# Performance work log

Measured on AMD Instinct MI355X. Metric: run time of the kernel, lower is better.

Reference implementation:

```python
import jax, jax.numpy as jnp
from jax import lax
import numpy as np

B, N, C = 4, 16384, 64
M_POINT, K_SAMPLE = 1024, 32
RADIUS = 0.5
LN_EPS = 1e-5
CP = C + 3  # grouped channels with use_xyz


def _fps(xyz, m):
    """D-FPS: furthest point sampling on Euclidean coords. xyz (B,N,3) -> (B,m) int32."""
    b, n, _ = xyz.shape
    min_d = jnp.full((b, n), 1e10, xyz.dtype)
    pt0 = xyz[:, 0]  # CUDA FPS starts from index 0

    def step(carry, _):
        md, last = carry
        d = jnp.sum((xyz - last[:, None, :]) ** 2, axis=-1)  # (B,N)
        md = jnp.minimum(md, d)
        idx = jnp.argmax(md, axis=1)  # (B,)
        nxt = jnp.take_along_axis(xyz, idx[:, None, None], axis=1)[:, 0]
        return (md, nxt), idx.astype(jnp.int32)

    _, idxs = lax.scan(step, (min_d, pt0), None, length=m - 1)  # (m-1,B)
    return jnp.concatenate([jnp.zeros((1, b), jnp.int32), idxs], axis=0).T  # (B,m)


def _ball_query(xyz, new_xyz, radius, k):
    """First k neighbors (by original index) within radius; pad with first hit. -> (B,M,k)."""
    b, n, _ = xyz.shape
    d2 = jnp.sum((new_xyz[:, :, None, :] - xyz[:, None, :, :]) ** 2, -1)  # (B,M,N)
    scores = jnp.where(d2 <= radius * radius, jnp.arange(n, dtype=jnp.int32), n)
    neg_top, _ = lax.top_k(-scores, k)  # k smallest scores = first k in-radius indices
    idx = -neg_top  # (B,M,k), ascending
    idx = jnp.where(idx < n, idx, idx[..., :1])  # pad invalid slots with first hit
    return idx


def setup_inputs() -> dict:
    key = jax.random.key(0)
    ks = jax.random.split(key, 8)
    points_xyz = jax.random.uniform(ks[0], (B, N, 3)) * 2.0 - 1.0
    features = jax.random.normal(ks[1], (B, C, N))
    prompt_emb = jax.random.normal(ks[2], (1, M_POINT, 2)) * 0.02
    proj_w = jax.random.normal(ks[3], (CP, 2)) * 0.5
    proj_b = jnp.zeros((CP,))
    ln_g = jnp.ones((CP,))
    ln_b = jnp.zeros((CP,))
    pw_w = jax.random.normal(ks[4], (M_POINT, CP)) * 0.05
    pw_b = jnp.zeros((M_POINT,))
    w0 = jax.random.normal(ks[5], (128, CP)) / np.sqrt(CP)
    b0 = jnp.zeros((128,))
    w1 = jax.random.normal(ks[6], (256, 128)) / np.sqrt(128.0)
    b1 = jnp.zeros((256,))
    return dict(points_xyz=points_xyz, features=features, prompt_emb=prompt_emb,
                proj_w=proj_w, proj_b=proj_b, ln_g=ln_g, ln_b=ln_b,
                pw_w=pw_w, pw_b=pw_b, w0=w0, b0=b0, w1=w1, b1=b1)


def reference(points_xyz, features, prompt_emb, proj_w, proj_b, ln_g, ln_b,
              pw_w, pw_b, w0, b0, w1, b1):
    # sample centers (D-FPS)
    indices = _fps(points_xyz, M_POINT)                                   # (B,M)
    new_xyz = jnp.take_along_axis(points_xyz, indices[:, :, None], axis=1)  # (B,M,3)
    # ball-query grouping + gather
    idx = _ball_query(points_xyz, new_xyz, RADIUS, K_SAMPLE)              # (B,M,K)
    gx = jax.vmap(lambda p, i: p[i])(points_xyz, idx)                     # (B,M,K,3)
    gx = gx - new_xyz[:, :, None, :]                                      # relative xyz
    gf = jax.vmap(lambda f, i: f[:, i])(features, idx)                    # (B,C,M,K)
    g = jnp.concatenate([jnp.transpose(gx, (0, 3, 1, 2)), gf], axis=1)    # (B,C+3,M,K)
    # incorporate_prompt
    emb = g.mean(axis=(-2, -1))                                           # (B,C+3)
    pw = jax.nn.softmax(emb @ pw_w.T + pw_b, axis=1)                      # (B,M)
    pe = prompt_emb @ proj_w.T + proj_b                                   # (1,M,C+3)
    mu = pe.mean(-1, keepdims=True)
    var = ((pe - mu) ** 2).mean(-1, keepdims=True)
    pe = (pe - mu) * lax.rsqrt(var + LN_EPS) * ln_g + ln_b
    pe = jax.nn.gelu(pe, approximate=False)                               # (1,M,C+3)
    g = g + pe[0].T[None, :, :, None] * pw[:, None, :, None]              # (B,C+3,M,K)
    # shared MLP (1x1 conv) + ReLU
    h = jax.nn.relu(jnp.einsum('oc,bcmk->bomk', w0, g) + b0[:, None, None])
    h = jax.nn.relu(jnp.einsum('oc,bcmk->bomk', w1, h) + b1[:, None, None])
    # max pool over neighbors K
    pooled = h.max(axis=-1)                                               # (B,256,M)
    return new_xyz, pooled, indices
```

## Files before the change

### kernel.cpp

```cpp
#include <hip/hip_runtime.h>
#include <hip/hip_bf16.h>

#define NB   4
#define NPTS 16384
#define NC   64
#define NM   1024
#define NK   32
#define NCP  67
#define RAD2 0.25f

#define OFF_W0T     0u
#define OFF_W1T     8576u
#define OFF_NEWXYZ  41344u
#define OFF_IDXBALL 53632u
#define OFF_CNT     184704u
#define OFF_EMB     250240u
#define OFF_PW      250624u
#define OFF_PE      254720u
#define OFF_SX      323328u
#define OFF_SY      388864u
#define OFF_SZ      454400u
#define OFF_SKLO    519936u

#define OUT_NEWXYZ 0u
#define OUT_POOLED 12288u
#define OUT_IDX    1060864u

__global__ __launch_bounds__(256) void k_prepw(const float* __restrict__ w0,
                                               const float* __restrict__ w1,
                                               float* __restrict__ w0t,
                                               float* __restrict__ w1t) {
  int t = blockIdx.x * 256 + threadIdx.x;
  if (t < 128 * NCP) { int o = t / NCP, c = t % NCP; w0t[c * 128 + o] = w0[t]; }
  if (t < 256 * 128) { int o2 = t / 128, o = t % 128; w1t[o * 256 + o2] = w1[t]; }
}

__device__ __forceinline__ unsigned mpart3(unsigned v) {
  return (v & 1u) | ((v & 2u) << 2) | ((v & 4u) << 4);
}
__device__ __forceinline__ unsigned cellof(float x, float y, float z) {
  unsigned qx = (unsigned)fminf(fmaxf((x + 1.0f) * 4.0f, 0.0f), 7.0f);
  unsigned qy = (unsigned)fminf(fmaxf((y + 1.0f) * 4.0f, 0.0f), 7.0f);
  unsigned qz = (unsigned)fminf(fmaxf((z + 1.0f) * 4.0f, 0.0f), 7.0f);
  return mpart3(qx) | (mpart3(qy) << 1) | (mpart3(qz) << 2);
}

__global__ __launch_bounds__(1024) void k_sort(const float* __restrict__ xyz,
                                               float* __restrict__ sx,
                                               float* __restrict__ sy,
                                               float* __restrict__ sz,
                                               unsigned* __restrict__ sklo) {
  const int b = blockIdx.x, t = threadIdx.x;
  const int lane = t & 63, wid = t >> 6;
  const float* xb = xyz + (size_t)b * NPTS * 3;
  __shared__ unsigned s_hist[512], s_off[512], s_wsum[8];
  if (t < 512) s_hist[t] = 0u;
  __syncthreads();
#pragma unroll
  for (int i = 0; i < 16; ++i) {
    int p = t + 1024 * i;
    float x = xb[p * 3 + 0], y = xb[p * 3 + 1], z = xb[p * 3 + 2];
    atomicAdd(&s_hist[cellof(x, y, z)], 1u);
  }
  __syncthreads();
  unsigned v = (t < 512) ? s_hist[t] : 0u;
#pragma unroll
  for (int off = 1; off < 64; off <<= 1) {
    unsigned u = __shfl_up(v, off);
    if (lane >= off) v += u;
  }
  if (t < 512 && lane == 63) s_wsum[wid] = v;
  __syncthreads();
  if (t < 512) {
    unsigned add = 0;
    for (int w = 0; w < wid; ++w) add += s_wsum[w];
    s_off[t] = add + v - s_hist[t];
  }
  __syncthreads();
#pragma unroll
  for (int i = 0; i < 16; ++i) {
    int p = t + 1024 * i;
    float x = xb[p * 3 + 0], y = xb[p * 3 + 1], z = xb[p * 3 + 2];
    unsigned pos = atomicAdd(&s_off[cellof(x, y, z)], 1u);
    sx[b * NPTS + pos] = x;
    sy[b * NPTS + pos] = y;
    sz[b * NPTS + pos] = z;
    sklo[b * NPTS + pos] = 16383u - (unsigned)p;
  }
}

__device__ __forceinline__ unsigned long long umax64(unsigned long long a,
                                                     unsigned long long b) {
  return a > b ? a : b;
}
__device__ __forceinline__ unsigned long long pack_key(float m, unsigned kl,
                                                       int bb) {
  return (((unsigned long long)__float_as_uint(m)) << 22) |
         (((unsigned long long)kl) << 8) | (unsigned long long)(unsigned)bb;
}

template <bool INIT>
__device__ __forceinline__ void fps_bucket(
    int bbp, int gl, float lx, float ly, float lz,
    const float* __restrict__ bx, const float* __restrict__ by,
    const float* __restrict__ bz, const unsigned* __restrict__ bk,
    float* s_md, unsigned short* s_klo,
    unsigned long long* skey_out, float4* swin_out,
    float* s_bxl, float* s_bxh, float* s_byl, float* s_byh,
    float* s_bzl, float* s_bzh) {
  const int p0 = bbp * 64 + gl * 8;
  float4 xa = *(const float4*)(bx + p0);
  float4 xc = *(const float4*)(bx + p0 + 4);
  float4 ya = *(const float4*)(by + p0);
  float4 yc = *(const float4*)(by + p0 + 4);
  float4 za = *(const float4*)(bz + p0);
  float4 zc = *(const float4*)(bz + p0 + 4);
  float xx[8] = {xa.x, xa.y, xa.z, xa.w, xc.x, xc.y, xc.z, xc.w};
  float yy[8] = {ya.x, ya.y, ya.z, ya.w, yc.x, yc.y, yc.z, yc.w};
  float zz[8] = {za.x, za.y, za.z, za.w, zc.x, zc.y, zc.z, zc.w};
  unsigned kls[8];
  float mds[8];
  if constexpr (INIT) {
    uint4 k0 = *(const uint4*)(bk + p0);
    uint4 k1 = *(const uint4*)(bk + p0 + 4);
    kls[0] = k0.x; kls[1] = k0.y; kls[2] = k0.z; kls[3] = k0.w;
    kls[4] = k1.x; kls[5] = k1.y; kls[6] = k1.z; kls[7] = k1.w;
  } else {
    uint4 kv = *(const uint4*)(&s_klo[p0]);
    kls[0] = kv.x & 0xFFFFu; kls[1] = kv.x >> 16;
    kls[2] = kv.y & 0xFFFFu; kls[3] = kv.y >> 16;
    kls[4] = kv.z & 0xFFFFu; kls[5] = kv.z >> 16;
    kls[6] = kv.w & 0xFFFFu; kls[7] = kv.w >> 16;
    float4 ma = *(const float4*)(&s_md[p0]);
    float4 mb = *(const float4*)(&s_md[p0 + 4]);
    mds[0] = ma.x; mds[1] = ma.y; mds[2] = ma.z; mds[3] = ma.w;
    mds[4] = mb.x; mds[5] = mb.y; mds[6] = mb.z; mds[7] = mb.w;
  }
  unsigned long long best = 0ull;
  float bwx = 0.f, bwy = 0.f, bwz = 0.f;
  float nmd[8];
#pragma unroll
  for (int i = 0; i < 8; ++i) {
    float dx = __fsub_rn(xx[i], lx);
    float dy = __fsub_rn(yy[i], ly);
    float dz = __fsub_rn(zz[i], lz);
    float d2 = __fadd_rn(__fadd_rn(__fmul_rn(dx, dx), __fmul_rn(dy, dy)),
                         __fmul_rn(dz, dz));
    float m = INIT ? d2 : fminf(mds[i], d2);
    nmd[i] = m;
    unsigned long long key = pack_key(m, kls[i], bbp);
    if (key > best) { best = key; bwx = xx[i]; bwy = yy[i]; bwz = zz[i]; }
  }
  *(float4*)(&s_md[p0])     = make_float4(nmd[0], nmd[1], nmd[2], nmd[3]);
  *(float4*)(&s_md[p0 + 4]) = make_float4(nmd[4], nmd[5], nmd[6], nmd[7]);
  if constexpr (INIT) {
    uint4 kw;
    kw.x = kls[0] | (kls[1] << 16); kw.y = kls[2] | (kls[3] << 16);
    kw.z = kls[4] | (kls[5] << 16); kw.w = kls[6] | (kls[7] << 16);
    *(uint4*)(&s_klo[p0]) = kw;
  }
  unsigned long long gk = best;
#pragma unroll
  for (int off = 1; off < 8; off <<= 1) {
    unsigned long long o = __shfl_xor(gk, off);
    gk = o > gk ? o : gk;
  }
  if constexpr (INIT) {
    float xl = xx[0], xh = xx[0], yl = yy[0], yh = yy[0], zl = zz[0], zh = zz[0];
#pragma unroll
    for (int i = 1; i < 8; ++i) {
      xl = fminf(xl, xx[i]); xh = fmaxf(xh, xx[i]);
      yl = fminf(yl, yy[i]); yh = fmaxf(yh, yy[i]);
      zl = fminf(zl, zz[i]); zh = fmaxf(zh, zz[i]);
    }
#pragma unroll
    for (int off = 1; off < 8; off <<= 1) {
      xl = fminf(xl, __shfl_xor(xl, off)); xh = fmaxf(xh, __shfl_xor(xh, off));
      yl = fminf(yl, __shfl_xor(yl, off)); yh = fmaxf(yh, __shfl_xor(yh, off));
      zl = fminf(zl, __shfl_xor(zl, off)); zh = fmaxf(zh, __shfl_xor(zh, off));
    }
    if (gl == 0) {
      s_bxl[bbp] = xl; s_bxh[bbp] = xh;
      s_byl[bbp] = yl; s_byh[bbp] = yh;
      s_bzl[bbp] = zl; s_bzh[bbp] = zh;
    }
  }
  if (best == gk) swin_out[bbp] = make_float4(bwx, bwy, bwz, 0.f);
  if (gl == 0) skey_out[bbp] = gk;
}

__global__ __launch_bounds__(512) void k_fps(const float* __restrict__ xyz,
                                             const float* __restrict__ sx,
                                             const float* __restrict__ sy,
                                             const float* __restrict__ sz,
                                             const unsigned* __restrict__ sklo,
                                             float* __restrict__ newxyz,
                                             float* __restrict__ out) {
  const int b = blockIdx.x, t = threadIdx.x;
  const int lane = t & 63, w = t >> 6;
  const int gl = lane & 7, g = lane >> 3;
  const float* xb = xyz + (size_t)b * NPTS * 3;
  const float* bx = sx + b * NPTS;
  const float* by = sy + b * NPTS;
  const float* bz = sz + b * NPTS;
  const unsigned* bk = sklo + b * NPTS;
  __shared__ float s_md[NPTS];
  __shared__ unsigned short s_klo[NPTS];
  __shared__ float s_bxl[256], s_bxh[256], s_byl[256], s_byh[256],
                   s_bzl[256], s_bzh[256];
  __shared__ unsigned long long s_bkey[2][256];
  __shared__ float4 s_bwin[2][256];
  float lx = xb[0], ly = xb[1], lz = xb[2];
  if (t == 0) {
    newxyz[(size_t)b * NM * 3 + 0] = lx;
    newxyz[(size_t)b * NM * 3 + 1] = ly;
    newxyz[(size_t)b * NM * 3 + 2] = lz;
    out[OUT_NEWXYZ + (size_t)b * NM * 3 + 0] = lx;
    out[OUT_NEWXYZ + (size_t)b * NM * 3 + 1] = ly;
    out[OUT_NEWXYZ + (size_t)b * NM * 3 + 2] = lz;
    out[OUT_IDX + b * NM] = 0.0f;
  }
#pragma unroll
  for (int r = 0; r < 4; ++r) {
    int bbp = 32 * w + r * 8 + g;
    fps_bucket<true>(bbp, gl, lx, ly, lz, bx, by, bz, bk, s_md, s_klo,
                     s_bkey[0], s_bwin[0],
                     s_bxl, s_bxh, s_byl, s_byh, s_bzl, s_bzh);
  }
  __syncthreads();
  for (int s = 1; s < NM; ++s) {
    const int cur = s & 1, prv = cur ^ 1;
    unsigned long long k =
        umax64(umax64(s_bkey[prv][lane], s_bkey[prv][lane + 64]),
               umax64(s_bkey[prv][lane + 128], s_bkey[prv][lane + 192]));
#pragma unroll
    for (int off = 1; off < 64; off <<= 1) {
      unsigned long long o = __shfl_xor(k, off);
      k = o > k ? o : k;
    }
    const int bbw = (int)(k & 0xFFull);
    float4 wv = s_bwin[prv][bbw];
    lx = wv.x; ly = wv.y; lz = wv.z;
    if (t == 0) {
      const int idx = 16383 - (int)((k >> 8) & 0x3FFFull);
      newxyz[((size_t)b * NM + s) * 3 + 0] = lx;
      newxyz[((size_t)b * NM + s) * 3 + 1] = ly;
      newxyz[((size_t)b * NM + s) * 3 + 2] = lz;
      out[OUT_NEWXYZ + ((size_t)b * NM + s) * 3 + 0] = lx;
      out[OUT_NEWXYZ + ((size_t)b * NM + s) * 3 + 1] = ly;
      out[OUT_NEWXYZ + ((size_t)b * NM + s) * 3 + 2] = lz;
      out[OUT_IDX + b * NM + s] = (float)idx;
    }
    bool keep = false;
    if (lane < 32) {
      const int bbj = 32 * w + lane;
      unsigned long long kj = s_bkey[prv][bbj];
      float mm = __uint_as_float((unsigned)(kj >> 22));
      float gx = fmaxf(fmaxf(__fsub_rn(s_bxl[bbj], lx), __fsub_rn(lx, s_bxh[bbj])), 0.f);
      float gy = fmaxf(fmaxf(__fsub_rn(s_byl[bbj], ly), __fsub_rn(ly, s_byh[bbj])), 0.f);
      float gz = fmaxf(fmaxf(__fsub_rn(s_bzl[bbj], lz), __fsub_rn(lz, s_bzh[bbj])), 0.f);
      float lb = __fadd_rn(__fadd_rn(__fmul_rn(gx, gx), __fmul_rn(gy, gy)),
                           __fmul_rn(gz, gz));
      keep = !(__fmul_rn(lb, 0.999984741f) > __fmul_rn(mm, 1.000015259f));
      if (!keep) {
        s_bkey[cur][bbj] = kj;
        s_bwin[cur][bbj] = s_bwin[prv][bbj];
      }
    }
    unsigned long long mask = __ballot(keep);
    while (mask) {
      unsigned long long m2 = mask;
#pragma unroll
      for (int r = 0; r < 7; ++r) if (r < g) m2 &= (m2 - 1ull);
      if (m2) {
        int jj = (int)__builtin_ctzll(m2);
        fps_bucket<false>(32 * w + jj, gl, lx, ly, lz, bx, by, bz, bk,
                          s_md, s_klo, s_bkey[cur], s_bwin[cur],
                          s_bxl, s_bxh, s_byl, s_byh, s_bzl, s_bzh);
      }
#pragma unroll
      for (int r = 0; r < 8; ++r) mask &= (mask - 1ull);
    }
    __syncthreads();
  }
}

__global__ __launch_bounds__(256) void k_ball(const float* __restrict__ xyz,
                                              const float* __restrict__ newxyz,
                                              int* __restrict__ idxball,
                                              int* __restrict__ cnt,
                                              float* __restrict__ emb) {
  __shared__ int s_idx[4][NK];
  const int lane = threadIdx.x & 63, wid = threadIdx.x >> 6;
  const int gid = blockIdx.x * 4 + wid;
  const int b = gid >> 10;
  const float* xb = xyz + (size_t)b * NPTS * 3;
  const float cx = newxyz[gid * 3 + 0];
  const float cy = newxyz[gid * 3 + 1];
  const float cz = newxyz[gid * 3 + 2];
  int total = 0;
  for (int base = 0; base < NPTS && total < NK; base += 64) {
    int n = base + lane;
    float dx = __fsub_rn(xb[n * 3 + 0], cx);
    float dy = __fsub_rn(xb[n * 3 + 1], cy);
    float dz = __fsub_rn(xb[n * 3 + 2], cz);
    float d2 = __fadd_rn(__fadd_rn(__fmul_rn(dx, dx), __fmul_rn(dy, dy)),
                         __fmul_rn(dz, dz));
    bool hit = d2 <= RAD2;
    unsigned long long mask = __ballot(hit);
    int pos = total + (int)__popcll(mask & ((1ull << lane) - 1ull));
    if (hit && pos < NK) s_idx[wid][pos] = n;
    total += (int)__popcll(mask);
  }
  int tt = total < NK ? total : NK;
  if (lane >= tt && lane < NK) s_idx[wid][lane] = s_idx[wid][0];
  int v = 0;
  if (lane < NK) {
    v = s_idx[wid][lane];
    idxball[(size_t)gid * NK + lane] = v;
    atomicAdd(&cnt[b * NPTS + v], 1);
  }
  float sx = 0.f, sy = 0.f, sz = 0.f;
  if (lane < NK) { sx = xb[v * 3 + 0]; sy = xb[v * 3 + 1]; sz = xb[v * 3 + 2]; }
#pragma unroll
  for (int off = 1; off < 64; off <<= 1) {
    sx += __shfl_xor(sx, off);
    sy += __shfl_xor(sy, off);
    sz += __shfl_xor(sz, off);
  }
  if (lane == 0) {
    atomicAdd(&emb[b * 96 + 0], sx - 32.0f * cx);
    atomicAdd(&emb[b * 96 + 1], sy - 32.0f * cy);
    atomicAdd(&emb[b * 96 + 2], sz - 32.0f * cz);
  }
}

__global__ __launch_bounds__(256) void k_embfeat(const float* __restrict__ feat,
                                                 const int* __restrict__ cnt,
                                                 float* __restrict__ emb) {
  const int c = blockIdx.x, b = blockIdx.y;
  const float* f = feat + ((size_t)b * NC + c) * NPTS;
  const int* ct = cnt + b * NPTS;
  float acc = 0.f;
  for (int n = threadIdx.x; n < NPTS; n += 256)
    acc = fmaf((float)ct[n], f[n], acc);
  __shared__ float red[4];
#pragma unroll
  for (int off = 1; off < 64; off <<= 1) acc += __shfl_xor(acc, off);
  if ((threadIdx.x & 63) == 0) red[threadIdx.x >> 6] = acc;
  __syncthreads();
  if (threadIdx.x == 0)
    emb[b * 96 + 3 + c] = red[0] + red[1] + red[2] + red[3];
}

__global__ __launch_bounds__(64) void k_pe(const float* __restrict__ prompt,
                                           const float* __restrict__ projw,
                                           const float* __restrict__ projb,
                                           const float* __restrict__ lng,
                                           const float* __restrict__ lnb,
                                           float* __restrict__ pe) {
  const int m = blockIdx.x, lane = threadIdx.x;
  const float p0 = prompt[m * 2 + 0], p1 = prompt[m * 2 + 1];
  const int c1 = lane, c2 = lane + 64;
  float v1 = p0 * projw[c1 * 2 + 0] + p1 * projw[c1 * 2 + 1] + projb[c1];
  float v2 = 0.f;
  if (c2 < NCP) v2 = p0 * projw[c2 * 2 + 0] + p1 * projw[c2 * 2 + 1] + projb[c2];
  float s = v1 + ((c2 < NCP) ? v2 : 0.f);
#pragma unroll
  for (int off = 1; off < 64; off <<= 1) s += __shfl_xor(s, off);
  float mu = s * (1.0f / 67.0f);
  float d1 = v1 - mu;
  float d2v = (c2 < NCP) ? (v2 - mu) : 0.f;
  float q = d1 * d1 + d2v * d2v;
#pragma unroll
  for (int off = 1; off < 64; off <<= 1) q += __shfl_xor(q, off);
  float inv = 1.0f / sqrtf(q * (1.0f / 67.0f) + 1e-5f);
  {
    float y = d1 * inv * lng[c1] + lnb[c1];
    pe[m * NCP + c1] = 0.5f * y * (1.0f + erff(y * 0.70710678118654752f));
  }
  if (c2 < NCP) {
    float y = (v2 - mu) * inv * lng[c2] + lnb[c2];
    pe[m * NCP + c2] = 0.5f * y * (1.0f + erff(y * 0.70710678118654752f));
  }
}

__global__ __launch_bounds__(1024) void k_pw(const float* __restrict__ emb,
                                             const float* __restrict__ pww,
                                             const float* __restrict__ pwb,
                                             float* __restrict__ pw) {
  const int b = blockIdx.x, m = threadIdx.x;
  __shared__ float se[NCP];
  __shared__ float red[16];
  __shared__ float bcast;
  if (m < NCP) se[m] = emb[b * 96 + m] * (1.0f / 32768.0f);
  __syncthreads();
  float acc = pwb[m];
  for (int c = 0; c < NCP; ++c) acc = fmaf(se[c], pww[m * NCP + c], acc);
  float mx = acc;
#pragma unroll
  for (int off = 1; off < 64; off <<= 1) mx = fmaxf(mx, __shfl_xor(mx, off));
  if ((m & 63) == 0) red[m >> 6] = mx;
  __syncthreads();
  if (m == 0) {
    float v = red[0];
    for (int w = 1; w < 16; ++w) v = fmaxf(v, red[w]);
    bcast = v;
  }
  __syncthreads();
  float e = expf(acc - bcast);
  float ssum = e;
#pragma unroll
  for (int off = 1; off < 64; off <<= 1) ssum += __shfl_xor(ssum, off);
  if ((m & 63) == 0) red[m >> 6] = ssum;
  __syncthreads();
  if (m == 0) {
    float v = 0.f;
    for (int w = 0; w < 16; ++w) v += red[w];
    bcast = v;
  }
  __syncthreads();
  pw[b * NM + m] = e / bcast;
}

__global__ __launch_bounds__(256) void k_main(const float* __restrict__ feat,
                                              const float* __restrict__ xyz,
                                              const float* __restrict__ newxyz,
                                              const int* __restrict__ idxball,
                                              const float* __restrict__ pe,
                                              const float* __restrict__ pwbuf,
                                              const float* __restrict__ w0t,
                                              const float* __restrict__ b0,
                                              const float* __restrict__ w1t,
                                              const float* __restrict__ b1,
                                              float* __restrict__ out) {
  __shared__ __align__(16) float g[NCP * 36];
  __shared__ __align__(16) float h0[128 * 36];
  __shared__ int s_idx[NK];
  __shared__ float spe[NCP];
  const int bid = blockIdx.x;
  const int b = bid >> 10, m = bid & 1023;
  const int t = threadIdx.x;
  const float pwv = pwbuf[bid];
  if (t < NK) {
    int n = idxball[(size_t)bid * NK + t];
    n = n < 0 ? 0 : (n > NPTS - 1 ? NPTS - 1 : n);
    s_idx[t] = n;
  }
  if (t < NCP) spe[t] = pe[m * NCP + t] * pwv;
  __syncthreads();
  for (int e = t; e < NK * NC; e += 256) {
    int k = e >> 6, c = e & 63;
    int n = s_idx[k];
    g[(3 + c) * 36 + k] = feat[((size_t)b * NC + c) * NPTS + n] + spe[3 + c];
  }
  if (t < 96) {
    int k = t & 31, d = t >> 5;
    int n = s_idx[k];
    float cv = newxyz[bid * 3 + d];
    g[d * 36 + k] = (xyz[((size_t)b * NPTS + n) * 3 + d] - cv) + spe[d];
  }
  __syncthreads();
  {
    const int o = t & 127, kb = (t >> 7) * 16;
    float acc[16];
    float bb = b0[o];
#pragma unroll
    for (int j = 0; j < 16; ++j) acc[j] = bb;
    for (int c = 0; c < NCP; ++c) {
      float w = w0t[c * 128 + o];
      const float4* gp = reinterpret_cast<const float4*>(&g[c * 36 + kb]);
#pragma unroll
      for (int qq = 0; qq < 4; ++qq) {
        float4 gv = gp[qq];
        acc[qq * 4 + 0] = fmaf(w, gv.x, acc[qq * 4 + 0]);
        acc[qq * 4 + 1] = fmaf(w, gv.y, acc[qq * 4 + 1]);
        acc[qq * 4 + 2] = fmaf(w, gv.z, acc[qq * 4 + 2]);
        acc[qq * 4 + 3] = fmaf(w, gv.w, acc[qq * 4 + 3]);
      }
    }
    float4* hp = reinterpret_cast<float4*>(&h0[o * 36 + kb]);
#pragma unroll
    for (int qq = 0; qq < 4; ++qq) {
      float4 hv;
      hv.x = fmaxf(acc[qq * 4 + 0], 0.f);
      hv.y = fmaxf(acc[qq * 4 + 1], 0.f);
      hv.z = fmaxf(acc[qq * 4 + 2], 0.f);
      hv.w = fmaxf(acc[qq * 4 + 3], 0.f);
      hp[qq] = hv;
    }
  }
  __syncthreads();
  {
    const int o2 = t;
    float acc[32];
    float bb = b1[o2];
#pragma unroll
    for (int j = 0; j < 32; ++j) acc[j] = bb;
    for (int o = 0; o < 128; ++o) {
      float w = w1t[o * 256 + o2];
      const float4* hp = reinterpret_cast<const float4*>(&h0[o * 36]);
#pragma unroll
      for (int qq = 0; qq < 8; ++qq) {
        float4 hv = hp[qq];
        acc[qq * 4 + 0] = fmaf(w, hv.x, acc[qq * 4 + 0]);
        acc[qq * 4 + 1] = fmaf(w, hv.y, acc[qq * 4 + 1]);
        acc[qq * 4 + 2] = fmaf(w, hv.z, acc[qq * 4 + 2]);
        acc[qq * 4 + 3] = fmaf(w, hv.w, acc[qq * 4 + 3]);
      }
    }
    float mx = 0.f;
#pragma unroll
    for (int k = 0; k < 32; ++k) mx = fmaxf(mx, acc[k]);
    out[OUT_POOLED + ((size_t)(b * 256 + o2)) * NM + m] = mx;
  }
}

extern "C" void kernel_launch(void* const* d_in, const int* in_sizes, int n_in,
                              void* d_out, int out_size, void* d_ws, size_t ws_size,
                              hipStream_t stream) {
  const float* xyz    = (const float*)d_in[0];
  const float* feat   = (const float*)d_in[1];
  const float* prompt = (const float*)d_in[2];
  const float* projw  = (const float*)d_in[3];
  const float* projb  = (const float*)d_in[4];
  const float* lng    = (const float*)d_in[5];
  const float* lnb    = (const float*)d_in[6];
  const float* pww    = (const float*)d_in[7];
  const float* pwb    = (const float*)d_in[8];
  const float* w0     = (const float*)d_in[9];
  const float* b0     = (const float*)d_in[10];
  const float* w1     = (const float*)d_in[11];
  const float* b1     = (const float*)d_in[12];
  float* ws = (float*)d_ws;
  float* out = (float*)d_out;

  float* w0t      = ws + OFF_W0T;
  float* w1t      = ws + OFF_W1T;
  float* nxyz     = ws + OFF_NEWXYZ;
  int*   idxball  = (int*)(ws + OFF_IDXBALL);
  int*   cnt      = (int*)(ws + OFF_CNT);
  float* emb      = ws + OFF_EMB;
  float* pwv      = ws + OFF_PW;
  float* pev      = ws + OFF_PE;
  float* sxw      = ws + OFF_SX;
  float* syw      = ws + OFF_SY;
  float* szw      = ws + OFF_SZ;
  unsigned* sklo  = (unsigned*)(ws + OFF_SKLO);

  hipMemsetAsync(cnt, 0, NB * NPTS * sizeof(int), stream);
  hipMemsetAsync(emb, 0, NB * 96 * sizeof(float), stream);

  k_prepw<<<128, 256, 0, stream>>>(w0, w1, w0t, w1t);
  k_sort<<<NB, 1024, 0, stream>>>(xyz, sxw, syw, szw, sklo);
  k_fps<<<NB, 512, 0, stream>>>(xyz, sxw, syw, szw, sklo, nxyz, out);
  k_ball<<<NB * NM / 4, 256, 0, stream>>>(xyz, nxyz, idxball, cnt, emb);
  k_embfeat<<<dim3(NC, NB), 256, 0, stream>>>(feat, cnt, emb);
  k_pe<<<NM, 64, 0, stream>>>(prompt, projw, projb, lng, lnb, pev);
  k_pw<<<NB, 1024, 0, stream>>>(emb, pww, pwb, pwv);
  k_main<<<NB * NM, 256, 0, stream>>>(feat, xyz, nxyz, idxball, pev, pwv,
                                      w0t, b0, w1t, b1, out);
}
```

Measured before the change: 2.433 ms.

## Use 16-lane bucket groups with DPP reductions in FPS and cache bucket bounds in registers

The FPS bucket update now assigns 16 lanes of 4 points each to a bucket instead of 8 lanes of 8 points. The intra-group argmax, including the winning coordinates, and the bounding-box min/max are reduced with DPP row_shr operations instead of __shfl_xor. The wave-wide key max also moves to DPP row shifts and broadcasts plus readlane. Each lane keeps its bucket's bounding box in registers rather than reloading it from LDS every step. The goal is to cut shuffle latency and per-lane serial work on the serial FPS critical path. The cost is fewer buckets processed in parallel per wave pass and DPP code that is harder to get right, for example with row masks.

```diff
diff --git a/kernel.cpp b/kernel.cpp
--- a/kernel.cpp
+++ b/kernel.cpp
@@ -99,94 +99,118 @@
          (((unsigned long long)kl) << 8) | (unsigned long long)(unsigned)bb;
 }
 
+#define DPPI(v, CTRL, RM) \
+  __builtin_amdgcn_update_dpp((int)(v), (int)(v), CTRL, RM, 0xf, false)
+
+#define DPP_PAY(CTRL) { \
+  unsigned h2 = (unsigned)DPPI(hi, CTRL, 0xf); \
+  unsigned l2 = (unsigned)DPPI(lo, CTRL, 0xf); \
+  float x2 = __int_as_float(DPPI(__float_as_int(bwx), CTRL, 0xf)); \
+  float y2 = __int_as_float(DPPI(__float_as_int(bwy), CTRL, 0xf)); \
+  float z2 = __int_as_float(DPPI(__float_as_int(bwz), CTRL, 0xf)); \
+  bool tk = (h2 > hi) || (h2 == hi && l2 > lo); \
+  hi = tk ? h2 : hi; lo = tk ? l2 : lo; \
+  bwx = tk ? x2 : bwx; bwy = tk ? y2 : bwy; bwz = tk ? z2 : bwz; }
+
+#define DPP_K(CTRL, RM) { \
+  unsigned h2 = (unsigned)DPPI(hi, CTRL, RM); \
+  unsigned l2 = (unsigned)DPPI(lo, CTRL, RM); \
+  bool tk = (h2 > hi) || (h2 == hi && l2 > lo); \
+  hi = tk ? h2 : hi; lo = tk ? l2 : lo; }
+
+#define DPP_FMIN(v, CTRL) v = fminf(v, __int_as_float(DPPI(__float_as_int(v), CTRL, 0xf)));
+#define DPP_FMAX(v, CTRL) v = fmaxf(v, __int_as_float(DPPI(__float_as_int(v), CTRL, 0xf)));
+
+__device__ __forceinline__ unsigned long long wave_max_key(unsigned long long k) {
+  unsigned hi = (unsigned)(k >> 32), lo = (unsigned)k;
+  DPP_K(0x111, 0xf)
+  DPP_K(0x112, 0xf)
+  DPP_K(0x114, 0xf)
+  DPP_K(0x118, 0xf)
+  DPP_K(0x142, 0xa)
+  DPP_K(0x143, 0xc)
+  hi = (unsigned)__builtin_amdgcn_readlane((int)hi, 63);
+  lo = (unsigned)__builtin_amdgcn_readlane((int)lo, 63);
+  return ((unsigned long long)hi << 32) | lo;
+}
+
 template <bool INIT>
-__device__ __forceinline__ void fps_bucket(
-    int bbp, int gl, float lx, float ly, float lz,
+__device__ __forceinline__ void fps_bucket16(
+    int bbp, int rl, float lx, float ly, float lz,
     const float* __restrict__ bx, const float* __restrict__ by,
     const float* __restrict__ bz, const unsigned* __restrict__ bk,
     float* s_md, unsigned short* s_klo,
     unsigned long long* skey_out, float4* swin_out,
     float* s_bxl, float* s_bxh, float* s_byl, float* s_byh,
     float* s_bzl, float* s_bzh) {
-  const int p0 = bbp * 64 + gl * 8;
-  float4 xa = *(const float4*)(bx + p0);
-  float4 xc = *(const float4*)(bx + p0 + 4);
-  float4 ya = *(const float4*)(by + p0);
-  float4 yc = *(const float4*)(by + p0 + 4);
-  float4 za = *(const float4*)(bz + p0);
-  float4 zc = *(const float4*)(bz + p0 + 4);
-  float xx[8] = {xa.x, xa.y, xa.z, xa.w, xc.x, xc.y, xc.z, xc.w};
-  float yy[8] = {ya.x, ya.y, ya.z, ya.w, yc.x, yc.y, yc.z, yc.w};
-  float zz[8] = {za.x, za.y, za.z, za.w, zc.x, zc.y, zc.z, zc.w};
-  unsigned kls[8];
-  float mds[8];
+  const int p0 = bbp * 64 + rl * 4;
+  float4 xv = *(const float4*)(bx + p0);
+  float4 yv = *(const float4*)(by + p0);
+  float4 zv = *(const float4*)(bz + p0);
+  float xs[4] = {xv.x, xv.y, xv.z, xv.w};
+  float ys[4] = {yv.x, yv.y, yv.z, yv.w};
+  float zs[4] = {zv.x, zv.y, zv.z, zv.w};
+  unsigned kl[4];
+  float md0[4];
   if constexpr (INIT) {
-    uint4 k0 = *(const uint4*)(bk + p0);
-    uint4 k1 = *(const uint4*)(bk + p0 + 4);
-    kls[0] = k0.x; kls[1] = k0.y; kls[2] = k0.z; kls[3] = k0.w;
-    kls[4] = k1.x; kls[5] = k1.y; kls[6] = k1.z; kls[7] = k1.w;
+    uint4 kk = *(const uint4*)(bk + p0);
+    kl[0] = kk.x; kl[1] = kk.y; kl[2] = kk.z; kl[3] = kk.w;
   } else {
-    uint4 kv = *(const uint4*)(&s_klo[p0]);
-    kls[0] = kv.x & 0xFFFFu; kls[1] = kv.x >> 16;
-    kls[2] = kv.y & 0xFFFFu; kls[3] = kv.y >> 16;
-    kls[4] = kv.z & 0xFFFFu; kls[5] = kv.z >> 16;
-    kls[6] = kv.w & 0xFFFFu; kls[7] = kv.w >> 16;
-    float4 ma = *(const float4*)(&s_md[p0]);
-    float4 mb = *(const float4*)(&s_md[p0 + 4]);
-    mds[0] = ma.x; mds[1] = ma.y; mds[2] = ma.z; mds[3] = ma.w;
-    mds[4] = mb.x; mds[5] = mb.y; mds[6] = mb.z; mds[7] = mb.w;
-  }
-  unsigned long long best = 0ull;
+    uint2 kk = *(const uint2*)(&s_klo[p0]);
+    kl[0] = kk.x & 0xFFFFu; kl[1] = kk.x >> 16;
+    kl[2] = kk.y & 0xFFFFu; kl[3] = kk.y >> 16;
+    float4 mv = *(const float4*)(&s_md[p0]);
+    md0[0] = mv.x; md0[1] = mv.y; md0[2] = mv.z; md0[3] = mv.w;
+  }
+  unsigned hi = 0u, lo = 0u;
   float bwx = 0.f, bwy = 0.f, bwz = 0.f;
-  float nmd[8];
-#pragma unroll
-  for (int i = 0; i < 8; ++i) {
-    float dx = __fsub_rn(xx[i], lx);
-    float dy = __fsub_rn(yy[i], ly);
-    float dz = __fsub_rn(zz[i], lz);
+  float nm[4];
+#pragma unroll
+  for (int i = 0; i < 4; ++i) {
+    float dx = __fsub_rn(xs[i], lx);
+    float dy = __fsub_rn(ys[i], ly);
+    float dz = __fsub_rn(zs[i], lz);
     float d2 = __fadd_rn(__fadd_rn(__fmul_rn(dx, dx), __fmul_rn(dy, dy)),
                          __fmul_rn(dz, dz));
-    float m = INIT ? d2 : fminf(mds[i], d2);
-    nmd[i] = m;
-    unsigned long long key = pack_key(m, kls[i], bbp);
-    if (key > best) { best = key; bwx = xx[i]; bwy = yy[i]; bwz = zz[i]; }
-  }
-  *(float4*)(&s_md[p0])     = make_float4(nmd[0], nmd[1], nmd[2], nmd[3]);
-  *(float4*)(&s_md[p0 + 4]) = make_float4(nmd[4], nmd[5], nmd[6], nmd[7]);
+    float m = INIT ? d2 : fminf(md0[i], d2);
+    nm[i] = m;
+    unsigned long long key = pack_key(m, kl[i], bbp);
+    unsigned h = (unsigned)(key >> 32), l = (unsigned)key;
+    bool tk = (h > hi) || (h == hi && l > lo);
+    hi = tk ? h : hi; lo = tk ? l : lo;
+    bwx = tk ? xs[i] : bwx; bwy = tk ? ys[i] : bwy; bwz = tk ? zs[i] : bwz;
+  }
+  *(float4*)(&s_md[p0]) = make_float4(nm[0], nm[1], nm[2], nm[3]);
   if constexpr (INIT) {
-    uint4 kw;
-    kw.x = kls[0] | (kls[1] << 16); kw.y = kls[2] | (kls[3] << 16);
-    kw.z = kls[4] | (kls[5] << 16); kw.w = kls[6] | (kls[7] << 16);
-    *(uint4*)(&s_klo[p0]) = kw;
-  }
-  unsigned long long gk = best;
-#pragma unroll
-  for (int off = 1; off < 8; off <<= 1) {
-    unsigned long long o = __shfl_xor(gk, off);
-    gk = o > gk ? o : gk;
-  }
+    uint2 kw;
+    kw.x = kl[0] | (kl[1] << 16);
+    kw.y = kl[2] | (kl[3] << 16);
+    *(uint2*)(&s_klo[p0]) = kw;
+  }
+  DPP_PAY(0x111) DPP_PAY(0x112) DPP_PAY(0x114) DPP_PAY(0x118)
   if constexpr (INIT) {
-    float xl = xx[0], xh = xx[0], yl = yy[0], yh = yy[0], zl = zz[0], zh = zz[0];
-#pragma unroll
-    for (int i = 1; i < 8; ++i) {
-      xl = fminf(xl, xx[i]); xh = fmaxf(xh, xx[i]);
-      yl = fminf(yl, yy[i]); yh = fmaxf(yh, yy[i]);
-      zl = fminf(zl, zz[i]); zh = fmaxf(zh, zz[i]);
-    }
-#pragma unroll
-    for (int off = 1; off < 8; off <<= 1) {
-      xl = fminf(xl, __shfl_xor(xl, off)); xh = fmaxf(xh, __shfl_xor(xh, off));
-      yl = fminf(yl, __shfl_xor(yl, off)); yh = fmaxf(yh, __shfl_xor(yh, off));
-      zl = fminf(zl, __shfl_xor(zl, off)); zh = fmaxf(zh, __shfl_xor(zh, off));
-    }
-    if (gl == 0) {
+    float xl = fminf(fminf(xs[0], xs[1]), fminf(xs[2], xs[3]));
+    float xh = fmaxf(fmaxf(xs[0], xs[1]), fmaxf(xs[2], xs[3]));
+    float yl = fminf(fminf(ys[0], ys[1]), fminf(ys[2], ys[3]));
+    float yh = fmaxf(fmaxf(ys[0], ys[1]), fmaxf(ys[2], ys[3]));
+    float zl = fminf(fminf(zs[0], zs[1]), fminf(zs[2], zs[3]));
+    float zh = fmaxf(fmaxf(zs[0], zs[1]), fmaxf(zs[2], zs[3]));
+    DPP_FMIN(xl, 0x111) DPP_FMIN(xl, 0x112) DPP_FMIN(xl, 0x114) DPP_FMIN(xl, 0x118)
+    DPP_FMAX(xh, 0x111) DPP_FMAX(xh, 0x112) DPP_FMAX(xh, 0x114) DPP_FMAX(xh, 0x118)
+    DPP_FMIN(yl, 0x111) DPP_FMIN(yl, 0x112) DPP_FMIN(yl, 0x114) DPP_FMIN(yl, 0x118)
+    DPP_FMAX(yh, 0x111) DPP_FMAX(yh, 0x112) DPP_FMAX(yh, 0x114) DPP_FMAX(yh, 0x118)
+    DPP_FMIN(zl, 0x111) DPP_FMIN(zl, 0x112) DPP_FMIN(zl, 0x114) DPP_FMIN(zl, 0x118)
+    DPP_FMAX(zh, 0x111) DPP_FMAX(zh, 0x112) DPP_FMAX(zh, 0x114) DPP_FMAX(zh, 0x118)
+    if (rl == 15) {
       s_bxl[bbp] = xl; s_bxh[bbp] = xh;
       s_byl[bbp] = yl; s_byh[bbp] = yh;
       s_bzl[bbp] = zl; s_bzh[bbp] = zh;
     }
   }
-  if (best == gk) swin_out[bbp] = make_float4(bwx, bwy, bwz, 0.f);
-  if (gl == 0) skey_out[bbp] = gk;
+  if (rl == 15) {
+    skey_out[bbp] = ((unsigned long long)hi << 32) | lo;
+    swin_out[bbp] = make_float4(bwx, bwy, bwz, 0.f);
+  }
 }
 
 __global__ __launch_bounds__(512) void k_fps(const float* __restrict__ xyz,
@@ -198,7 +222,7 @@
                                              float* __restrict__ out) {
   const int b = blockIdx.x, t = threadIdx.x;
   const int lane = t & 63, w = t >> 6;
-  const int gl = lane & 7, g = lane >> 3;
+  const int rl = lane & 15, g4 = lane >> 4;
   const float* xb = xyz + (size_t)b * NPTS * 3;
   const float* bx = sx + b * NPTS;
   const float* by = sy + b * NPTS;
@@ -221,11 +245,18 @@
     out[OUT_IDX + b * NM] = 0.0f;
   }
 #pragma unroll
-  for (int r = 0; r < 4; ++r) {
-    int bbp = 32 * w + r * 8 + g;
-    fps_bucket<true>(bbp, gl, lx, ly, lz, bx, by, bz, bk, s_md, s_klo,
-                     s_bkey[0], s_bwin[0],
-                     s_bxl, s_bxh, s_byl, s_byh, s_bzl, s_bzh);
+  for (int r = 0; r < 8; ++r) {
+    int bbp = 32 * w + r * 4 + g4;
+    fps_bucket16<true>(bbp, rl, lx, ly, lz, bx, by, bz, bk, s_md, s_klo,
+                       s_bkey[0], s_bwin[0],
+                       s_bxl, s_bxh, s_byl, s_byh, s_bzl, s_bzh);
+  }
+  float rxl = 0.f, rxh = 0.f, ryl = 0.f, ryh = 0.f, rzl = 0.f, rzh = 0.f;
+  if (lane < 32) {
+    int bbj = 32 * w + lane;
+    rxl = s_bxl[bbj]; rxh = s_bxh[bbj];
+    ryl = s_byl[bbj]; ryh = s_byh[bbj];
+    rzl = s_bzl[bbj]; rzh = s_bzh[bbj];
   }
   __syncthreads();
   for (int s = 1; s < NM; ++s) {
@@ -233,11 +264,7 @@
     unsigned long long k =
         umax64(umax64(s_bkey[prv][lane], s_bkey[prv][lane + 64]),
                umax64(s_bkey[prv][lane + 128], s_bkey[prv][lane + 192]));
-#pragma unroll
-    for (int off = 1; off < 64; off <<= 1) {
-      unsigned long long o = __shfl_xor(k, off);
-      k = o > k ? o : k;
-    }
+    k = wave_max_key(k);
     const int bbw = (int)(k & 0xFFull);
     float4 wv = s_bwin[prv][bbw];
     lx = wv.x; ly = wv.y; lz = wv.z;
@@ -256,9 +283,9 @@
       const int bbj = 32 * w + lane;
       unsigned long long kj = s_bkey[prv][bbj];
       float mm = __uint_as_float((unsigned)(kj >> 22));
-      float gx = fmaxf(fmaxf(__fsub_rn(s_bxl[bbj], lx), __fsub_rn(lx, s_bxh[bbj])), 0.f);
-      float gy = fmaxf(fmaxf(__fsub_rn(s_byl[bbj], ly), __fsub_rn(ly, s_byh[bbj])), 0.f);
-      float gz = fmaxf(fmaxf(__fsub_rn(s_bzl[bbj], lz), __fsub_rn(lz, s_bzh[bbj])), 0.f);
+      float gx = fmaxf(fmaxf(__fsub_rn(rxl, lx), __fsub_rn(lx, rxh)), 0.f);
+      float gy = fmaxf(fmaxf(__fsub_rn(ryl, ly), __fsub_rn(ly, ryh)), 0.f);
+      float gz = fmaxf(fmaxf(__fsub_rn(rzl, lz), __fsub_rn(lz, rzh)), 0.f);
       float lb = __fadd_rn(__fadd_rn(__fmul_rn(gx, gx), __fmul_rn(gy, gy)),
                            __fmul_rn(gz, gz));
       keep = !(__fmul_rn(lb, 0.999984741f) > __fmul_rn(mm, 1.000015259f));
@@ -271,15 +298,15 @@
     while (mask) {
       unsigned long long m2 = mask;
 #pragma unroll
-      for (int r = 0; r < 7; ++r) if (r < g) m2 &= (m2 - 1ull);
+      for (int r = 0; r < 3; ++r) if (r < g4) m2 &= (m2 - 1ull);
       if (m2) {
         int jj = (int)__builtin_ctzll(m2);
-        fps_bucket<false>(32 * w + jj, gl, lx, ly, lz, bx, by, bz, bk,
-                          s_md, s_klo, s_bkey[cur], s_bwin[cur],
-                          s_bxl, s_bxh, s_byl, s_byh, s_bzl, s_bzh);
+        fps_bucket16<false>(32 * w + jj, rl, lx, ly, lz, bx, by, bz, bk,
+                            s_md, s_klo, s_bkey[cur], s_bwin[cur],
+                            s_bxl, s_bxh, s_byl, s_byh, s_bzl, s_bzh);
       }
 #pragma unroll
-      for (int r = 0; r < 8; ++r) mask &= (mask - 1ull);
+      for (int r = 0; r < 4; ++r) mask &= (mask - 1ull);
     }
     __syncthreads();
   }
```

Result: slower. 2.939 ms (+20.8%).
